# Kernel tuning notes

Measured on AMD Instinct MI355X. Metric: run time of the kernel, lower is better.

Reference implementation:

```python
import jax, jax.numpy as jnp
import numpy as np

N, E, D, H, G = 100000, 1250000, 64, 64, 128
GRAPH_ATTR_DIM = 4
BN_EPS = 1e-5


def setup_inputs() -> dict:
    key = jax.random.key(0)
    ks = jax.random.split(key, 32)
    inp = {
        "x": jax.random.normal(ks[0], (N, D), dtype=jnp.float32),
        "edge_index": jax.random.randint(ks[1], (2, E), 0, N, dtype=jnp.int64),
        "batch": jnp.sort(jax.random.randint(ks[2], (N,), 0, G, dtype=jnp.int64)),
        "graph_attr": jax.random.normal(ks[3], (G, GRAPH_ATTR_DIM), dtype=jnp.float32),
    }
    # SAGEConv params per layer: lin_l (neighbor path, with bias), lin_r (self path, no bias)
    dims = [(D, H), (H, H), (H, H)]
    kidx = 4
    for i, (din, dout) in enumerate(dims):
        s = 1.0 / np.sqrt(din)
        inp[f"Wl{i}"] = jax.random.uniform(ks[kidx + 0], (din, dout), minval=-s, maxval=s, dtype=jnp.float32)
        inp[f"bl{i}"] = jax.random.uniform(ks[kidx + 1], (dout,), minval=-s, maxval=s, dtype=jnp.float32)
        inp[f"Wr{i}"] = jax.random.uniform(ks[kidx + 2], (din, dout), minval=-s, maxval=s, dtype=jnp.float32)
        # BatchNorm1d (eval mode: running stats)
        inp[f"g{i}"] = jnp.ones((dout,), jnp.float32)
        inp[f"be{i}"] = jnp.zeros((dout,), jnp.float32)
        inp[f"rm{i}"] = jax.random.normal(ks[kidx + 3], (dout,), dtype=jnp.float32) * 0.1
        inp[f"rv{i}"] = jax.random.uniform(ks[kidx + 4], (dout,), minval=0.5, maxval=1.5, dtype=jnp.float32)
        kidx += 5
    clf_in, clf_h = H + GRAPH_ATTR_DIM, H // 2
    s1 = 1.0 / np.sqrt(clf_in)
    s2 = 1.0 / np.sqrt(clf_h)
    inp["W1"] = jax.random.uniform(ks[kidx + 0], (clf_in, clf_h), minval=-s1, maxval=s1, dtype=jnp.float32)
    inp["b1"] = jax.random.uniform(ks[kidx + 1], (clf_h,), minval=-s1, maxval=s1, dtype=jnp.float32)
    inp["W2"] = jax.random.uniform(ks[kidx + 2], (clf_h, 2), minval=-s2, maxval=s2, dtype=jnp.float32)
    inp["b2"] = jax.random.uniform(ks[kidx + 3], (2,), minval=-s2, maxval=s2, dtype=jnp.float32)
    return inp


def _sage_conv(x, src, dst, Wl, bl, Wr):
    # mean-aggregate neighbor messages x[src] onto dst nodes
    msg = x[src]                                            # [E, d]
    agg = jax.ops.segment_sum(msg, dst, num_segments=N)     # [N, d]
    cnt = jax.ops.segment_sum(jnp.ones((src.shape[0],), x.dtype), dst, num_segments=N)
    agg = agg / jnp.maximum(cnt, 1.0)[:, None]
    return agg @ Wl + bl + x @ Wr


def _bn_eval(x, g, be, rm, rv):
    return (x - rm) * (g * jax.lax.rsqrt(rv + BN_EPS)) + be


def reference(x, edge_index, batch, graph_attr,
              Wl0, bl0, Wr0, g0, be0, rm0, rv0,
              Wl1, bl1, Wr1, g1, be1, rm1, rv1,
              Wl2, bl2, Wr2, g2, be2, rm2, rv2,
              W1, b1, W2, b2):
    src, dst = edge_index[0], edge_index[1]
    layer_params = [
        (Wl0, bl0, Wr0, g0, be0, rm0, rv0),
        (Wl1, bl1, Wr1, g1, be1, rm1, rv1),
        (Wl2, bl2, Wr2, g2, be2, rm2, rv2),
    ]
    h = x
    for (Wl, bl, Wr, g, be, rm, rv) in layer_params:
        h = jax.nn.relu(_bn_eval(_sage_conv(h, src, dst, Wl, bl, Wr), g, be, rm, rv))
        # dropout is identity in eval mode
    # global mean pool over graphs
    gsum = jax.ops.segment_sum(h, batch, num_segments=G)
    gcnt = jax.ops.segment_sum(jnp.ones((h.shape[0],), h.dtype), batch, num_segments=G)
    gemb = gsum / jnp.maximum(gcnt, 1.0)[:, None]
    gemb = jnp.concatenate([gemb, graph_attr], axis=1)      # [G, H+4]
    return jax.nn.relu(gemb @ W1 + b1) @ W2 + b2             # [G, 2]
```

## Files before the change

### kernel.cpp

```cpp
#include <hip/hip_runtime.h>
#include <hip/hip_fp16.h>

#define DIM 64
#define NGRAPH 128
#define GATTR 4
#define BN_EPS 1e-5f
#define SCAN_CHUNK 4096
#define SCHUNK 4096
#define BUCKET_SHIFT 7
#define BUCKET 128
#define XS 17


__global__ __launch_bounds__(256) void k_zero(float* __restrict__ gsum,
                                              int* __restrict__ gcnt) {
    int i0 = blockIdx.x * 256 + threadIdx.x;
    if (i0 < NGRAPH * DIM) gsum[i0] = 0.f;
    if (i0 < NGRAPH) gcnt[i0] = 0;
}


__global__ __launch_bounds__(256) void k_cast(const float4* __restrict__ x4,
                                              uint2* __restrict__ o, int n4) {
    int stride = gridDim.x * 256;
    for (int i = blockIdx.x * 256 + threadIdx.x; i < n4; i += stride) {
        float4 v = x4[i];
        __half2 a = __float22half2_rn(make_float2(v.x, v.y));
        __half2 b = __float22half2_rn(make_float2(v.z, v.w));
        uint2 u;
        u.x = *(unsigned int*)&a;
        u.y = *(unsigned int*)&b;
        o[i] = u;
    }
}


__global__ __launch_bounds__(256) void k_bhist(const int* __restrict__ dst,
                                               int* __restrict__ hist,
                                               int E, int nb, int nbuck) {
    __shared__ int lb[1024];
    int tid = threadIdx.x, blk = blockIdx.x;
    int base = blk * SCHUNK;
    int cnt = min(SCHUNK, E - base);
    for (int i = tid; i < nbuck; i += 256) lb[i] = 0;
    __syncthreads();
    for (int i = tid; i < cnt; i += 256)
        atomicAdd(&lb[dst[base + i] >> BUCKET_SHIFT], 1);
    __syncthreads();
    for (int b = tid; b < nbuck; b += 256) hist[b * nb + blk] = lb[b];
}

__global__ __launch_bounds__(256) void k_gscan1(const int* __restrict__ in,
                                                int* __restrict__ out,
                                                int* __restrict__ partials, int n) {
    __shared__ int ws[256];
    int tid = threadIdx.x;
    int base = blockIdx.x * SCAN_CHUNK + tid * 16;
    int v[16];
    int s = 0;
#pragma unroll
    for (int i = 0; i < 16; ++i) {
        int idx = base + i;
        v[i] = (idx < n) ? in[idx] : 0;
        s += v[i];
    }
    ws[tid] = s;
    __syncthreads();
    for (int off = 1; off < 256; off <<= 1) {
        int t = (tid >= off) ? ws[tid - off] : 0;
        __syncthreads();
        ws[tid] += t;
        __syncthreads();
    }
    int excl = (tid == 0) ? 0 : ws[tid - 1];
    if (tid == 255) partials[blockIdx.x] = ws[255];
#pragma unroll
    for (int i = 0; i < 16; ++i) {
        int idx = base + i;
        if (idx < n) out[idx] = excl;
        excl += v[i];
    }
}

__global__ __launch_bounds__(256) void k_gscan23(int* __restrict__ data,
                                                 const int* __restrict__ partials,
                                                 int n) {
    __shared__ int soff;
    if (threadIdx.x == 0) {
        int s = 0;
        for (int j = 0; j < blockIdx.x; ++j) s += partials[j];
        soff = s;
    }
    __syncthreads();
    int off = soff;
    int base = blockIdx.x * SCAN_CHUNK;
    for (int i = threadIdx.x; i < SCAN_CHUNK; i += 256) {
        int idx = base + i;
        if (idx < n) data[idx] += off;
    }
}

__global__ __launch_bounds__(256) void k_sbin(const int* __restrict__ src,
                                              const int* __restrict__ dst,
                                              const int* __restrict__ hist,
                                              int2* __restrict__ pairs,
                                              int E, int nb, int nbuck) {
    __shared__ int lhist[1024];
    __shared__ int lofs[1024];
    __shared__ int lcur[1024];
    __shared__ int lgb[1024];
    __shared__ int ws[256];
    __shared__ int2 stage[SCHUNK];
    int tid = threadIdx.x, blk = blockIdx.x;
    int base = blk * SCHUNK;
    int cnt = min(SCHUNK, E - base);

    for (int i = tid; i < nbuck; i += 256) lhist[i] = 0;
    __syncthreads();

    int2 mine[16];
    int nmine = 0;
    for (int i = tid; i < cnt; i += 256) {
        int s = src[base + i];
        int d = dst[base + i];
        mine[nmine++] = make_int2(s, d);
        atomicAdd(&lhist[d >> BUCKET_SHIFT], 1);
    }
    __syncthreads();

    {
        int b0 = tid * 4;
        int v0 = (b0 + 0 < nbuck) ? lhist[b0 + 0] : 0;
        int v1 = (b0 + 1 < nbuck) ? lhist[b0 + 1] : 0;
        int v2 = (b0 + 2 < nbuck) ? lhist[b0 + 2] : 0;
        int v3 = (b0 + 3 < nbuck) ? lhist[b0 + 3] : 0;
        int s = v0 + v1 + v2 + v3;
        ws[tid] = s;
        __syncthreads();
        for (int off = 1; off < 256; off <<= 1) {
            int t = (tid >= off) ? ws[tid - off] : 0;
            __syncthreads();
            ws[tid] += t;
            __syncthreads();
        }
        int excl = (tid == 0) ? 0 : ws[tid - 1];
        if (b0 + 0 < nbuck) lofs[b0 + 0] = excl;
        excl += v0;
        if (b0 + 1 < nbuck) lofs[b0 + 1] = excl;
        excl += v1;
        if (b0 + 2 < nbuck) lofs[b0 + 2] = excl;
        excl += v2;
        if (b0 + 3 < nbuck) lofs[b0 + 3] = excl;
    }
    __syncthreads();
    for (int b = tid; b < nbuck; b += 256) {
        lcur[b] = lofs[b];
        lgb[b] = hist[b * nb + blk];
    }
    __syncthreads();

    for (int j = 0; j < nmine; ++j) {
        int b = mine[j].y >> BUCKET_SHIFT;
        int pos = atomicAdd(&lcur[b], 1);
        stage[pos] = mine[j];
    }
    __syncthreads();

    for (int i = tid; i < cnt; i += 256) {
        int2 pr = stage[i];
        int b = pr.y >> BUCKET_SHIFT;
        pairs[lgb[b] + (i - lofs[b])] = pr;
    }
}

__global__ __launch_bounds__(256) void k_bsort(const int2* __restrict__ pairs,
                                               const int* __restrict__ hist,
                                               int* __restrict__ rowptr,
                                               int* __restrict__ col,
                                               int n, int nb, int nbuck, int E) {
    __shared__ int lcnt[BUCKET];
    __shared__ int lofs[BUCKET];
    int b = blockIdx.x;
    int tid = threadIdx.x;
    int cbase = hist[b * nb];
    int nxt = (b + 1 < nbuck) ? hist[(b + 1) * nb] : E;
    int ecnt = nxt - cbase;
    int node0 = b << BUCKET_SHIFT;
    int nn = min(BUCKET, n - node0);
    if (tid < BUCKET) lcnt[tid] = 0;
    __syncthreads();
    for (int i = tid; i < ecnt; i += 256)
        atomicAdd(&lcnt[pairs[cbase + i].y - node0], 1);
    __syncthreads();
    int v = (tid < BUCKET) ? lcnt[tid] : 0;
    if (tid < BUCKET) lofs[tid] = v;
    __syncthreads();
    for (int off = 1; off < BUCKET; off <<= 1) {
        int t = (tid < BUCKET && tid >= off) ? lofs[tid - off] : 0;
        __syncthreads();
        if (tid < BUCKET) lofs[tid] += t;
        __syncthreads();
    }
    int excl = (tid < BUCKET) ? (lofs[tid] - v) : 0;
    __syncthreads();
    if (tid < BUCKET) lofs[tid] = excl;
    if (tid < nn) rowptr[node0 + tid] = cbase + excl;
    __syncthreads();
    for (int i = tid; i < ecnt; i += 256) {
        int2 pr = pairs[cbase + i];
        int p = cbase + atomicAdd(&lofs[pr.y - node0], 1);
        col[p] = pr.x;
    }
    if (b == 0 && tid == 0) rowptr[n] = E;
}


__global__ __launch_bounds__(256) void k_agg(const __half* __restrict__ h16,
                                             const int* __restrict__ row_ptr,
                                             const int* __restrict__ col,
                                             float* __restrict__ agg, int n) {
    int wid = (blockIdx.x * blockDim.x + threadIdx.x) >> 6;
    if (wid >= n) return;
    int lane = threadIdx.x & 63;
    int g = lane >> 3;
    int p = lane & 7;
    int beg = row_ptr[wid], end = row_ptr[wid + 1];

    float a0 = 0.f, a1 = 0.f, a2 = 0.f, a3 = 0.f;
    float a4 = 0.f, a5 = 0.f, a6 = 0.f, a7 = 0.f;

#define ACCUM(V)                                                          \
    {                                                                     \
        const __half2* q = (const __half2*)&(V);                          \
        float2 f0 = __half22float2(q[0]);                                 \
        float2 f1 = __half22float2(q[1]);                                 \
        float2 f2 = __half22float2(q[2]);                                 \
        float2 f3 = __half22float2(q[3]);                                 \
        a0 += f0.x; a1 += f0.y; a2 += f1.x; a3 += f1.y;                   \
        a4 += f2.x; a5 += f2.y; a6 += f3.x; a7 += f3.y;                   \
    }

    int j = beg + g;
    for (; j + 8 < end; j += 16) {
        int s0 = col[j];
        int s1 = col[j + 8];
        uint4 v0 = ((const uint4*)(h16 + (size_t)s0 * DIM))[p];
        uint4 v1 = ((const uint4*)(h16 + (size_t)s1 * DIM))[p];
        ACCUM(v0)
        ACCUM(v1)
    }
    if (j < end) {
        int s0 = col[j];
        uint4 v0 = ((const uint4*)(h16 + (size_t)s0 * DIM))[p];
        ACCUM(v0)
    }
#undef ACCUM

#pragma unroll
    for (int m = 8; m <= 32; m <<= 1) {
        a0 += __shfl_xor(a0, m, 64);
        a1 += __shfl_xor(a1, m, 64);
        a2 += __shfl_xor(a2, m, 64);
        a3 += __shfl_xor(a3, m, 64);
        a4 += __shfl_xor(a4, m, 64);
        a5 += __shfl_xor(a5, m, 64);
        a6 += __shfl_xor(a6, m, 64);
        a7 += __shfl_xor(a7, m, 64);
    }

    if (g == 0) {
        float c = (float)(end - beg);
        float inv = 1.0f / fmaxf(c, 1.0f);
        float4* op = (float4*)(agg + (size_t)wid * DIM + p * 8);
        float4 r0, r1;
        r0.x = a0 * inv; r0.y = a1 * inv; r0.z = a2 * inv; r0.w = a3 * inv;
        r1.x = a4 * inv; r1.y = a5 * inv; r1.z = a6 * inv; r1.w = a7 * inv;
        op[0] = r0;
        op[1] = r1;
    }
}


__global__ __launch_bounds__(256) void k_xform(const float* __restrict__ agg,
                                               const __half* __restrict__ h16,
                                               const float* __restrict__ Wl,
                                               const float* __restrict__ bl,
                                               const float* __restrict__ Wr,
                                               const float* __restrict__ bng,
                                               const float* __restrict__ bnb,
                                               const float* __restrict__ bnm,
                                               const float* __restrict__ bnv,
                                               __half* __restrict__ out16, int n) {
    __shared__ float4 sWl[64 * 16];
    __shared__ float4 sWr[64 * 16];
    __shared__ float4 sA[64 * XS];
    __shared__ float4 sH[64 * XS];
    int tid = threadIdx.x;
    int base = blockIdx.x * 64;
    int rows = min(64, n - base);

    const float4* Wl4 = (const float4*)Wl;
    const float4* Wr4 = (const float4*)Wr;
    const float4* A4 = (const float4*)(agg + (size_t)base * DIM);
    const uint2* H2 = (const uint2*)(h16 + (size_t)base * DIM);
    for (int i = tid; i < 1024; i += 256) {
        sWl[i] = Wl4[i];
        sWr[i] = Wr4[i];
        int row = i >> 4, c = i & 15;
        float4 va = {0.f, 0.f, 0.f, 0.f}, vh = {0.f, 0.f, 0.f, 0.f};
        if (row < rows) {
            va = A4[i];
            uint2 u = H2[i];
            const __half2* q = (const __half2*)&u;
            float2 lo = __half22float2(q[0]);
            float2 hi = __half22float2(q[1]);
            vh.x = lo.x; vh.y = lo.y; vh.z = hi.x; vh.w = hi.y;
        }
        sA[row * XS + c] = va;
        sH[row * XS + c] = vh;
    }
    __syncthreads();

    int dq = tid & 15;
    int nq = tid >> 4;
    float4 acc0 = {0.f, 0.f, 0.f, 0.f};
    float4 acc1 = {0.f, 0.f, 0.f, 0.f};
    float4 acc2 = {0.f, 0.f, 0.f, 0.f};
    float4 acc3 = {0.f, 0.f, 0.f, 0.f};

    int arow = nq * 4 * XS;
#pragma unroll 4
    for (int kg = 0; kg < 16; ++kg) {
        float4 wl0 = sWl[(kg * 4 + 0) * 16 + dq];
        float4 wl1 = sWl[(kg * 4 + 1) * 16 + dq];
        float4 wl2 = sWl[(kg * 4 + 2) * 16 + dq];
        float4 wl3 = sWl[(kg * 4 + 3) * 16 + dq];
        float4 wr0 = sWr[(kg * 4 + 0) * 16 + dq];
        float4 wr1 = sWr[(kg * 4 + 1) * 16 + dq];
        float4 wr2 = sWr[(kg * 4 + 2) * 16 + dq];
        float4 wr3 = sWr[(kg * 4 + 3) * 16 + dq];
        float4 a0 = sA[arow + 0 * XS + kg];
        float4 a1 = sA[arow + 1 * XS + kg];
        float4 a2 = sA[arow + 2 * XS + kg];
        float4 a3 = sA[arow + 3 * XS + kg];
        float4 h0 = sH[arow + 0 * XS + kg];
        float4 h1 = sH[arow + 1 * XS + kg];
        float4 h2 = sH[arow + 2 * XS + kg];
        float4 h3 = sH[arow + 3 * XS + kg];
#define ACC1(AC, AV, HV)                                                        \
        AC.x += AV.x * wl0.x + AV.y * wl1.x + AV.z * wl2.x + AV.w * wl3.x       \
              + HV.x * wr0.x + HV.y * wr1.x + HV.z * wr2.x + HV.w * wr3.x;      \
        AC.y += AV.x * wl0.y + AV.y * wl1.y + AV.z * wl2.y + AV.w * wl3.y       \
              + HV.x * wr0.y + HV.y * wr1.y + HV.z * wr2.y + HV.w * wr3.y;      \
        AC.z += AV.x * wl0.z + AV.y * wl1.z + AV.z * wl2.z + AV.w * wl3.z       \
              + HV.x * wr0.z + HV.y * wr1.z + HV.z * wr2.z + HV.w * wr3.z;      \
        AC.w += AV.x * wl0.w + AV.y * wl1.w + AV.z * wl2.w + AV.w * wl3.w       \
              + HV.x * wr0.w + HV.y * wr1.w + HV.z * wr2.w + HV.w * wr3.w;
        ACC1(acc0, a0, h0)
        ACC1(acc1, a1, h1)
        ACC1(acc2, a2, h2)
        ACC1(acc3, a3, h3)
#undef ACC1
    }

    float4 g4 = ((const float4*)bng)[dq];
    float4 v4 = ((const float4*)bnv)[dq];
    float4 be4 = ((const float4*)bnb)[dq];
    float4 rm4 = ((const float4*)bnm)[dq];
    float4 bi4 = ((const float4*)bl)[dq];
    float4 sc;
    sc.x = g4.x / sqrtf(v4.x + BN_EPS);
    sc.y = g4.y / sqrtf(v4.y + BN_EPS);
    sc.z = g4.z / sqrtf(v4.z + BN_EPS);
    sc.w = g4.w / sqrtf(v4.w + BN_EPS);

    float4* accp[4] = {&acc0, &acc1, &acc2, &acc3};
#pragma unroll
    for (int i = 0; i < 4; ++i) {
        int node = base + nq * 4 + i;
        if (node < n) {
            float4 a = *accp[i];
            float4 r;
            r.x = fmaxf((a.x + bi4.x - rm4.x) * sc.x + be4.x, 0.f);
            r.y = fmaxf((a.y + bi4.y - rm4.y) * sc.y + be4.y, 0.f);
            r.z = fmaxf((a.z + bi4.z - rm4.z) * sc.z + be4.z, 0.f);
            r.w = fmaxf((a.w + bi4.w - rm4.w) * sc.w + be4.w, 0.f);
            __half2 o01 = __float22half2_rn(make_float2(r.x, r.y));
            __half2 o23 = __float22half2_rn(make_float2(r.z, r.w));
            uint2 u;
            u.x = *(unsigned int*)&o01;
            u.y = *(unsigned int*)&o23;
            ((uint2*)(out16 + (size_t)node * DIM))[dq] = u;
        }
    }
}


__global__ __launch_bounds__(256) void k_pool(const __half* __restrict__ h16,
                                              const int* __restrict__ batch,
                                              float* __restrict__ gsum,
                                              int* __restrict__ gcnt, int n) {
    int nw = gridDim.x * 4;
    int w = blockIdx.x * 4 + (threadIdx.x >> 6);
    int lane = threadIdx.x & 63;
    int chunk = (n + nw - 1) / nw;
    int s = w * chunk, e = min(s + chunk, n);
    if (s >= e) return;
    int cur = batch[s];
    float acc = 0.f;
    int cnt = 0;
    for (int i = s; i < e; ++i) {
        int g = batch[i];
        if (g != cur) {
            atomicAdd(&gsum[cur * DIM + lane], acc);
            if (lane == 0) atomicAdd(&gcnt[cur], cnt);
            acc = 0.f; cnt = 0; cur = g;
        }
        acc += __half2float(h16[(size_t)i * DIM + lane]);
        ++cnt;
    }
    atomicAdd(&gsum[cur * DIM + lane], acc);
    if (lane == 0) atomicAdd(&gcnt[cur], cnt);
}


__global__ __launch_bounds__(256) void k_mlp(const float* __restrict__ gsum,
                                             const int* __restrict__ gcnt,
                                             const float* __restrict__ gattr,
                                             const float* __restrict__ W1,
                                             const float* __restrict__ b1,
                                             const float* __restrict__ W2,
                                             const float* __restrict__ b2,
                                             float* __restrict__ out) {
    __shared__ float emb[NGRAPH][DIM + GATTR];
    __shared__ float hid[NGRAPH][32];
    int tid = threadIdx.x;
    for (int i = tid; i < NGRAPH * DIM; i += 256) {
        int g = i >> 6, d = i & 63;
        float c = (float)gcnt[g];
        emb[g][d] = gsum[i] / fmaxf(c, 1.0f);
    }
    for (int i = tid; i < NGRAPH * GATTR; i += 256) {
        int g = i >> 2, d = i & 3;
        emb[g][DIM + d] = gattr[i];
    }
    __syncthreads();
    for (int t = tid; t < NGRAPH * 32; t += 256) {
        int g = t >> 5, j = t & 31;
        float a = b1[j];
        for (int k = 0; k < DIM + GATTR; ++k) a += emb[g][k] * W1[k * 32 + j];
        hid[g][j] = fmaxf(a, 0.f);
    }
    __syncthreads();
    {
        int g = tid >> 1, o = tid & 1;
        float a = b2[o];
        for (int k = 0; k < 32; ++k) a += hid[g][k] * W2[k * 2 + o];
        out[g * 2 + o] = a;
    }
}

extern "C" void kernel_launch(void* const* d_in, const int* in_sizes, int n_in,
                              void* d_out, int out_size, void* d_ws, size_t ws_size,
                              hipStream_t stream) {
    const float* x = (const float*)d_in[0];
    const int* ei = (const int*)d_in[1];
    const int* batch = (const int*)d_in[2];
    const float* gattr = (const float*)d_in[3];
    const int N = in_sizes[0] / DIM;
    const int E = in_sizes[1] / 2;
    const int* src = ei;
    const int* dst = ei + E;

    const float *Wl[3], *bl[3], *Wr[3], *bg[3], *bb[3], *bm[3], *bv[3];
    for (int l = 0; l < 3; ++l) {
        int base = 4 + l * 7;
        Wl[l] = (const float*)d_in[base + 0];
        bl[l] = (const float*)d_in[base + 1];
        Wr[l] = (const float*)d_in[base + 2];
        bg[l] = (const float*)d_in[base + 3];
        bb[l] = (const float*)d_in[base + 4];
        bm[l] = (const float*)d_in[base + 5];
        bv[l] = (const float*)d_in[base + 6];
    }
    const float* W1 = (const float*)d_in[25];
    const float* b1 = (const float*)d_in[26];
    const float* W2 = (const float*)d_in[27];
    const float* b2 = (const float*)d_in[28];

    char* ws = (char*)d_ws;
    size_t off = 0;
    auto alloc = [&](size_t bytes) -> char* {
        char* p = ws + off;
        off += (bytes + 255) & ~(size_t)255;
        return p;
    };
    const int nb = (E + SCHUNK - 1) / SCHUNK;
    const int nbuck = (N + BUCKET - 1) >> BUCKET_SHIFT;
    const int total_h = nbuck * nb;

    int* rowptr = (int*)alloc((size_t)(N + 1) * 4);
    int* col = (int*)alloc((size_t)E * 4);
    int* hist = (int*)alloc((size_t)total_h * 4);
    float* aggb = (float*)alloc((size_t)N * DIM * 4);
    __half* x16 = (__half*)alloc((size_t)N * DIM * 2);
    __half* h16a = (__half*)alloc((size_t)N * DIM * 2);
    __half* h16b = (__half*)alloc((size_t)N * DIM * 2);
    float* gsum = (float*)alloc((size_t)NGRAPH * DIM * 4);
    int* gcnt = (int*)alloc((size_t)NGRAPH * 4);
    int* partials = (int*)alloc(1024 * 4);
    int2* pairs = (int2*)aggb;
    (void)ws_size;

    const int tpb = 256;
    const int nscanH = (total_h + SCAN_CHUNK - 1) / SCAN_CHUNK;

    k_zero<<<(NGRAPH * DIM + tpb - 1) / tpb, tpb, 0, stream>>>(gsum, gcnt);
    k_cast<<<1024, tpb, 0, stream>>>((const float4*)x, (uint2*)x16, N * DIM / 4);

    k_bhist<<<nb, tpb, 0, stream>>>(dst, hist, E, nb, nbuck);
    k_gscan1<<<nscanH, tpb, 0, stream>>>(hist, hist, partials, total_h);
    k_gscan23<<<nscanH, tpb, 0, stream>>>(hist, partials, total_h);
    k_sbin<<<nb, tpb, 0, stream>>>(src, dst, hist, pairs, E, nb, nbuck);
    k_bsort<<<nbuck, tpb, 0, stream>>>(pairs, hist, rowptr, col, N, nb, nbuck, E);

    const __half* hin = x16;
    __half* houts[3] = {h16a, h16b, h16a};
    for (int l = 0; l < 3; ++l) {
        k_agg<<<(N * 64 + tpb - 1) / tpb, tpb, 0, stream>>>(hin, rowptr, col, aggb, N);
        k_xform<<<(N + 63) / 64, 256, 0, stream>>>(aggb, hin, Wl[l], bl[l], Wr[l],
                                                   bg[l], bb[l], bm[l], bv[l], houts[l], N);
        hin = houts[l];
    }

    k_pool<<<256, tpb, 0, stream>>>(hin, batch, gsum, gcnt, N);
    k_mlp<<<1, tpb, 0, stream>>>(gsum, gcnt, gattr, W1, b1, W2, b2, (float*)d_out);
}
```

Before: 454.7 us.

## Fuse neighbor aggregation into layer transform kernel via shared memory

Merges the separate mean-aggregation kernel into the per-layer transform kernel. Each 64-node block's four wavefronts each gather and average 16 nodes' neighbor features straight into shared memory, so the fp32 aggregate buffer is no longer written to and reread from global memory and one launch per layer disappears. The cost is less parallelism in the gather: each block now gathers 64 nodes serially across 4 waves while also holding about 50KB of shared memory, which limits occupancy and latency hiding on the irregular gathers. The pairs buffer now gets its own workspace allocation instead of aliasing the removed aggregate buffer.

```diff
diff --git a/kernel.cpp b/kernel.cpp
--- a/kernel.cpp
+++ b/kernel.cpp
@@ -215,74 +215,9 @@
 }
 
 
-__global__ __launch_bounds__(256) void k_agg(const __half* __restrict__ h16,
-                                             const int* __restrict__ row_ptr,
-                                             const int* __restrict__ col,
-                                             float* __restrict__ agg, int n) {
-    int wid = (blockIdx.x * blockDim.x + threadIdx.x) >> 6;
-    if (wid >= n) return;
-    int lane = threadIdx.x & 63;
-    int g = lane >> 3;
-    int p = lane & 7;
-    int beg = row_ptr[wid], end = row_ptr[wid + 1];
-
-    float a0 = 0.f, a1 = 0.f, a2 = 0.f, a3 = 0.f;
-    float a4 = 0.f, a5 = 0.f, a6 = 0.f, a7 = 0.f;
-
-#define ACCUM(V)                                                          \
-    {                                                                     \
-        const __half2* q = (const __half2*)&(V);                          \
-        float2 f0 = __half22float2(q[0]);                                 \
-        float2 f1 = __half22float2(q[1]);                                 \
-        float2 f2 = __half22float2(q[2]);                                 \
-        float2 f3 = __half22float2(q[3]);                                 \
-        a0 += f0.x; a1 += f0.y; a2 += f1.x; a3 += f1.y;                   \
-        a4 += f2.x; a5 += f2.y; a6 += f3.x; a7 += f3.y;                   \
-    }
-
-    int j = beg + g;
-    for (; j + 8 < end; j += 16) {
-        int s0 = col[j];
-        int s1 = col[j + 8];
-        uint4 v0 = ((const uint4*)(h16 + (size_t)s0 * DIM))[p];
-        uint4 v1 = ((const uint4*)(h16 + (size_t)s1 * DIM))[p];
-        ACCUM(v0)
-        ACCUM(v1)
-    }
-    if (j < end) {
-        int s0 = col[j];
-        uint4 v0 = ((const uint4*)(h16 + (size_t)s0 * DIM))[p];
-        ACCUM(v0)
-    }
-#undef ACCUM
-
-#pragma unroll
-    for (int m = 8; m <= 32; m <<= 1) {
-        a0 += __shfl_xor(a0, m, 64);
-        a1 += __shfl_xor(a1, m, 64);
-        a2 += __shfl_xor(a2, m, 64);
-        a3 += __shfl_xor(a3, m, 64);
-        a4 += __shfl_xor(a4, m, 64);
-        a5 += __shfl_xor(a5, m, 64);
-        a6 += __shfl_xor(a6, m, 64);
-        a7 += __shfl_xor(a7, m, 64);
-    }
-
-    if (g == 0) {
-        float c = (float)(end - beg);
-        float inv = 1.0f / fmaxf(c, 1.0f);
-        float4* op = (float4*)(agg + (size_t)wid * DIM + p * 8);
-        float4 r0, r1;
-        r0.x = a0 * inv; r0.y = a1 * inv; r0.z = a2 * inv; r0.w = a3 * inv;
-        r1.x = a4 * inv; r1.y = a5 * inv; r1.z = a6 * inv; r1.w = a7 * inv;
-        op[0] = r0;
-        op[1] = r1;
-    }
-}
-
-
-__global__ __launch_bounds__(256) void k_xform(const float* __restrict__ agg,
-                                               const __half* __restrict__ h16,
+__global__ __launch_bounds__(256) void k_layer(const __half* __restrict__ h16in,
+                                               const int* __restrict__ row_ptr,
+                                               const int* __restrict__ col,
                                                const float* __restrict__ Wl,
                                                const float* __restrict__ bl,
                                                const float* __restrict__ Wr,
@@ -301,23 +236,79 @@
 
     const float4* Wl4 = (const float4*)Wl;
     const float4* Wr4 = (const float4*)Wr;
-    const float4* A4 = (const float4*)(agg + (size_t)base * DIM);
-    const uint2* H2 = (const uint2*)(h16 + (size_t)base * DIM);
+    const uint2* H2 = (const uint2*)(h16in + (size_t)base * DIM);
     for (int i = tid; i < 1024; i += 256) {
         sWl[i] = Wl4[i];
         sWr[i] = Wr4[i];
         int row = i >> 4, c = i & 15;
-        float4 va = {0.f, 0.f, 0.f, 0.f}, vh = {0.f, 0.f, 0.f, 0.f};
+        float4 vh = {0.f, 0.f, 0.f, 0.f};
         if (row < rows) {
-            va = A4[i];
             uint2 u = H2[i];
             const __half2* q = (const __half2*)&u;
             float2 lo = __half22float2(q[0]);
             float2 hi = __half22float2(q[1]);
             vh.x = lo.x; vh.y = lo.y; vh.z = hi.x; vh.w = hi.y;
         }
-        sA[row * XS + c] = va;
         sH[row * XS + c] = vh;
+    }
+
+    int lane = tid & 63;
+    int wv = tid >> 6;
+    int g = lane >> 3;
+    int p = lane & 7;
+    for (int t = 0; t < 16; ++t) {
+        int nd = wv * 16 + t;
+        int node = base + nd;
+        int beg = 0, end = 0;
+        if (node < n) { beg = row_ptr[node]; end = row_ptr[node + 1]; }
+
+        float a0 = 0.f, a1 = 0.f, a2 = 0.f, a3 = 0.f;
+        float a4 = 0.f, a5 = 0.f, a6 = 0.f, a7 = 0.f;
+#define ACCUM(V)                                                          \
+        {                                                                 \
+            const __half2* q = (const __half2*)&(V);                      \
+            float2 f0 = __half22float2(q[0]);                             \
+            float2 f1 = __half22float2(q[1]);                             \
+            float2 f2 = __half22float2(q[2]);                             \
+            float2 f3 = __half22float2(q[3]);                             \
+            a0 += f0.x; a1 += f0.y; a2 += f1.x; a3 += f1.y;               \
+            a4 += f2.x; a5 += f2.y; a6 += f3.x; a7 += f3.y;               \
+        }
+        int j = beg + g;
+        for (; j + 8 < end; j += 16) {
+            int s0 = col[j];
+            int s1 = col[j + 8];
+            uint4 v0 = ((const uint4*)(h16in + (size_t)s0 * DIM))[p];
+            uint4 v1 = ((const uint4*)(h16in + (size_t)s1 * DIM))[p];
+            ACCUM(v0)
+            ACCUM(v1)
+        }
+        if (j < end) {
+            int s0 = col[j];
+            uint4 v0 = ((const uint4*)(h16in + (size_t)s0 * DIM))[p];
+            ACCUM(v0)
+        }
+#undef ACCUM
+#pragma unroll
+        for (int m = 8; m <= 32; m <<= 1) {
+            a0 += __shfl_xor(a0, m, 64);
+            a1 += __shfl_xor(a1, m, 64);
+            a2 += __shfl_xor(a2, m, 64);
+            a3 += __shfl_xor(a3, m, 64);
+            a4 += __shfl_xor(a4, m, 64);
+            a5 += __shfl_xor(a5, m, 64);
+            a6 += __shfl_xor(a6, m, 64);
+            a7 += __shfl_xor(a7, m, 64);
+        }
+        if (g == 0) {
+            float c = (float)(end - beg);
+            float inv = 1.0f / fmaxf(c, 1.0f);
+            float4 r0, r1;
+            r0.x = a0 * inv; r0.y = a1 * inv; r0.z = a2 * inv; r0.w = a3 * inv;
+            r1.x = a4 * inv; r1.y = a5 * inv; r1.z = a6 * inv; r1.w = a7 * inv;
+            sA[nd * XS + 2 * p] = r0;
+            sA[nd * XS + 2 * p + 1] = r1;
+        }
     }
     __syncthreads();
 
@@ -502,14 +493,13 @@
     int* rowptr = (int*)alloc((size_t)(N + 1) * 4);
     int* col = (int*)alloc((size_t)E * 4);
     int* hist = (int*)alloc((size_t)total_h * 4);
-    float* aggb = (float*)alloc((size_t)N * DIM * 4);
+    int2* pairs = (int2*)alloc((size_t)E * 8);
     __half* x16 = (__half*)alloc((size_t)N * DIM * 2);
     __half* h16a = (__half*)alloc((size_t)N * DIM * 2);
     __half* h16b = (__half*)alloc((size_t)N * DIM * 2);
     float* gsum = (float*)alloc((size_t)NGRAPH * DIM * 4);
     int* gcnt = (int*)alloc((size_t)NGRAPH * 4);
     int* partials = (int*)alloc(1024 * 4);
-    int2* pairs = (int2*)aggb;
     (void)ws_size;
 
     const int tpb = 256;
@@ -527,8 +517,7 @@
     const __half* hin = x16;
     __half* houts[3] = {h16a, h16b, h16a};
     for (int l = 0; l < 3; ++l) {
-        k_agg<<<(N * 64 + tpb - 1) / tpb, tpb, 0, stream>>>(hin, rowptr, col, aggb, N);
-        k_xform<<<(N + 63) / 64, 256, 0, stream>>>(aggb, hin, Wl[l], bl[l], Wr[l],
+        k_layer<<<(N + 63) / 64, 256, 0, stream>>>(hin, rowptr, col, Wl[l], bl[l], Wr[l],
                                                    bg[l], bb[l], bm[l], bv[l], houts[l], N);
         hin = houts[l];
     }
```

Result: slower. 652.3 us (+43.5%).
